# Kernel tuning notes

Hardware: AMD Instinct MI355X
Metric: run time of the kernel (lower is better)

## Reference

```python
import jax, jax.numpy as jnp
from jax import lax
import numpy as np

B, S, D, COMP = 4, 1024, 512, 4


def setup_inputs() -> dict:
    key = jax.random.key(0)
    x = jax.random.normal(key, (B * S, D), dtype=jnp.float32)
    return {"x": x, "comp_rate": COMP, "seqlen": S}


def _merge_step(x, t, seq):
    # x: [seq, D], compacted so the k = seq - t valid tokens occupy rows 0..k-1.
    xn = jnp.roll(x, -1, axis=0)  # x[i+1] (wrap value never selected among valid pairs)
    # dist only feeds argmax (non-differentiable), mirror torch exactly; stop_gradient
    # keeps the vjp from saving residuals for this dead-for-gradients path.
    xg = lax.stop_gradient(x)
    dist = jnp.sum(xg * jnp.roll(xg, -1, axis=0), axis=-1)  # scalar_product metric
    j = jnp.arange(x.shape[0])
    dist = jnp.where(j < seq - 1 - t, dist, -jnp.inf)  # k-1 valid adjacent pairs
    mid = jnp.argmax(dist)
    jm = j[:, None]
    # rows < mid keep, row mid becomes (x[mid]+x[mid+1])/2, rows > mid shift left by 1
    return jnp.where(jm < mid, x, jnp.where(jm == mid, (x + xn) * 0.5, xn))


def _merge_sample(x, steps, seq):
    def body(carry, t):
        return _merge_step(carry, t, seq), None
    x, _ = lax.scan(body, x, jnp.arange(steps))
    return x


def reference(x, comp_rate, seqlen):
    d = x.shape[-1]
    b = x.shape[0] // seqlen
    n_comp = seqlen // comp_rate
    steps = seqlen - n_comp
    xb = x.reshape(b, seqlen, d)
    merged = jax.vmap(lambda xs: _merge_sample(xs, steps, seqlen))(xb)
    # torch smart_merge concatenates per-sample results along dim 0
    return merged[:, :n_comp].reshape(b * n_comp, d)
```

## Files before the change

kernel.cpp:

```cpp
#include <hip/hip_runtime.h>
#include <math.h>

#define S 1024
#define D 512
#define NCOMP (S / 4)
#define STEPS (S - NCOMP)
#define NEG_INF (-__builtin_inff())

__device__ __forceinline__ int   f2i(float x) { return __builtin_bit_cast(int, x); }
__device__ __forceinline__ float i2f(int x)   { return __builtin_bit_cast(float, x); }
__device__ __forceinline__ int   rfl(int x)   { return __builtin_amdgcn_readfirstlane(x); }

__device__ __forceinline__ unsigned fkey(float f) {
    unsigned u = __builtin_bit_cast(unsigned, f);
    return (u & 0x80000000u) ? ~u : (u | 0x80000000u);
}

__device__ __forceinline__ float wave_sum63(float x) {
    x += i2f(__builtin_amdgcn_update_dpp(0, f2i(x), 0x111, 0xF, 0xF, true));
    x += i2f(__builtin_amdgcn_update_dpp(0, f2i(x), 0x112, 0xF, 0xF, true));
    x += i2f(__builtin_amdgcn_update_dpp(0, f2i(x), 0x114, 0xF, 0xF, true));
    x += i2f(__builtin_amdgcn_update_dpp(0, f2i(x), 0x118, 0xF, 0xF, true));
    x += i2f(__builtin_amdgcn_update_dpp(0, f2i(x), 0x142, 0xA, 0xF, true));
    x += i2f(__builtin_amdgcn_update_dpp(0, f2i(x), 0x143, 0xC, 0xF, true));
    return x;
}

__device__ __forceinline__ unsigned wave_max63(unsigned x) {
#define MAXD(c, rm) { unsigned o_ = (unsigned)__builtin_amdgcn_update_dpp(0, (int)x, (c), (rm), 0xF, true); x = (x > o_) ? x : o_; }
    MAXD(0x111, 0xF) MAXD(0x112, 0xF) MAXD(0x114, 0xF)
    MAXD(0x118, 0xF) MAXD(0x142, 0xA) MAXD(0x143, 0xC)
#undef MAXD
    return x;
}

struct Row { float4 a, b; };

__device__ __forceinline__ Row row_load(const float* vals, int slot, int lane) {
    const float4* p = (const float4*)(vals + (size_t)slot * D);
    Row r; r.a = p[lane * 2]; r.b = p[lane * 2 + 1]; return r;
}
__device__ __forceinline__ void row_store(float* vals, int slot, int lane, Row r) {
    float4* p = (float4*)(vals + (size_t)slot * D);
    p[lane * 2] = r.a; p[lane * 2 + 1] = r.b;
}
__device__ __forceinline__ Row row_avg(Row x, Row y) {
    Row r;
    r.a.x = (x.a.x + y.a.x) * 0.5f; r.a.y = (x.a.y + y.a.y) * 0.5f;
    r.a.z = (x.a.z + y.a.z) * 0.5f; r.a.w = (x.a.w + y.a.w) * 0.5f;
    r.b.x = (x.b.x + y.b.x) * 0.5f; r.b.y = (x.b.y + y.b.y) * 0.5f;
    r.b.z = (x.b.z + y.b.z) * 0.5f; r.b.w = (x.b.w + y.b.w) * 0.5f;
    return r;
}
__device__ __forceinline__ float dot8_partial(Row x, Row y) {
    float acc = x.a.x * y.a.x;
    acc += x.a.y * y.a.y; acc += x.a.z * y.a.z; acc += x.a.w * y.a.w;
    acc += x.b.x * y.b.x; acc += x.b.y * y.b.y; acc += x.b.z * y.b.z; acc += x.b.w * y.b.w;
    return acc;
}
__device__ __forceinline__ int lsr(int s) { return ((unsigned)s < (unsigned)S) ? s : 0; }
__device__ __forceinline__ int lsl(int s) { return ((unsigned)s <= (unsigned)S) ? s : 0; }

__device__ __forceinline__ void tree16k(const unsigned (&av)[16], unsigned& cm, int& ca) {
    unsigned v8[8]; int k8[8];
#pragma unroll
    for (int k = 0; k < 8; ++k) { bool tk = av[k+8] > av[k]; v8[k] = tk ? av[k+8] : av[k]; k8[k] = tk ? (k+8) : k; }
    unsigned v4[4]; int k4[4];
#pragma unroll
    for (int k = 0; k < 4; ++k) { bool tk = v8[k+4] > v8[k]; v4[k] = tk ? v8[k+4] : v8[k]; k4[k] = tk ? k8[k+4] : k8[k]; }
    unsigned v2[2]; int k2[2];
#pragma unroll
    for (int k = 0; k < 2; ++k) { bool tk = v4[k+2] > v4[k]; v2[k] = tk ? v4[k+2] : v4[k]; k2[k] = tk ? k4[k+2] : k4[k]; }
    bool tk1 = v2[1] > v2[0];
    cm = tk1 ? v2[1] : v2[0];
    ca = tk1 ? k2[1] : k2[0];
}

__device__ __forceinline__ void upd(unsigned (&av)[16], int lane, int slot, unsigned key) {
    if (lane == (slot >> 4)) {
        switch (slot & 15) {
            case 0:  av[0]  = key; break;  case 1:  av[1]  = key; break;
            case 2:  av[2]  = key; break;  case 3:  av[3]  = key; break;
            case 4:  av[4]  = key; break;  case 5:  av[5]  = key; break;
            case 6:  av[6]  = key; break;  case 7:  av[7]  = key; break;
            case 8:  av[8]  = key; break;  case 9:  av[9]  = key; break;
            case 10: av[10] = key; break;  case 11: av[11] = key; break;
            case 12: av[12] = key; break;  case 13: av[13] = key; break;
            case 14: av[14] = key; break;  case 15: av[15] = key; break;
        }
    }
}

__global__ __launch_bounds__(256) void init_kernel(const float* __restrict__ x,
                                                   float* __restrict__ vals,
                                                   float* __restrict__ out) {
    const int blk = blockIdx.x, b = blk >> 4, g = blk & 15;
    const int tid = threadIdx.x, lane = tid & 63, w = tid >> 6;
    const float* xb = x + (size_t)b * S * D;
    if (vals != x) {
        float* vb = vals + (size_t)b * S * D;
        const float4* s4 = (const float4*)xb;
        float4* d4 = (float4*)vb;
        const int base = g * (S * D / 4 / 16);
        for (int i = tid; i < S * D / 4 / 16; i += 256) d4[base + i] = s4[base + i];
    }
    float* sd = out + (size_t)b * NCOMP * D;
#pragma unroll 1
    for (int j = 0; j < 16; ++j) {
        int pr = g * 64 + w * 16 + j;
        if (pr < S - 1) {
            Row A = row_load(xb, pr, lane);
            Row B = row_load(xb, pr + 1, lane);
            float t = wave_sum63(dot8_partial(A, B));
            if (lane == 63) sd[pr] = t;
        }
    }
    if (g == 0 && tid == 0) sd[S - 1] = NEG_INF;
}

__global__ __launch_bounds__(64, 1) void merge_kernel(float* __restrict__ vals,
                                                      float* __restrict__ out) {
    const int b = blockIdx.x, lane = threadIdx.x;
    float* vb = vals + (size_t)b * S * D;
    float* aux = out + (size_t)b * NCOMP * D;
    int* outIdx = (int*)(aux + S);

    __shared__ int4 links[S + 1];
    for (int s = lane; s <= S; s += 64)
        links[s] = (s >= S) ? make_int4(S, S, S, 0)
                            : make_int4(s - 1, s + 1, (s + 2 <= S) ? (s + 2) : S, 0);

    unsigned av[16];
    {
        const float4* sd4 = (const float4*)aux;
#pragma unroll
        for (int j = 0; j < 4; ++j) {
            float4 v = sd4[lane * 4 + j];
            av[4*j+0] = fkey(v.x); av[4*j+1] = fkey(v.y);
            av[4*j+2] = fkey(v.z); av[4*j+3] = fkey(v.w);
        }
    }

    unsigned cm; int ca;
    tree16k(av, cm, ca);
    unsigned smax = (unsigned)__builtin_amdgcn_readlane((int)wave_max63(cm), 63);
    unsigned long long tied = __ballot(cm == smax);
    int wl = (int)__ffsll(tied) - 1;
    int m = rfl((wl << 4) | __builtin_amdgcn_readlane(ca, wl));
    int4 Lm = links[m];
    int p = rfl(Lm.x), r = rfl(Lm.y), q = rfl(Lm.z);
    int nq = rfl(links[lsl(q)].y);
    Row Rp = row_load(vb, lsr(p), lane);
    Row Rm = row_load(vb, m,      lane);
    Row Rr = row_load(vb, r,      lane);
    Row Rq = row_load(vb, lsr(q), lane);
    int mprev = -1;
    Row vmPrev = Rm;

#pragma unroll 1
    for (int t = 0; ; ++t) {
        const bool hasp = (p >= 0), hasq = (q < S);
        if (p == mprev) Rp = vmPrev;
        if (m == mprev) Rm = vmPrev;
        if (r == mprev) Rr = vmPrev;
        if (q == mprev) Rq = vmPrev;

        Row vm = row_avg(Rm, Rr);
        row_store(vb, m, lane, vm);

        float sp = wave_sum63(dot8_partial(Rp, vm));
        float sq = wave_sum63(dot8_partial(vm, Rq));
        unsigned ndpk = hasp ? fkey(i2f(__builtin_amdgcn_readlane(f2i(sp), 63))) : 0u;
        unsigned ndmk = hasq ? fkey(i2f(__builtin_amdgcn_readlane(f2i(sq), 63))) : 0u;

        if (lane == 0) {
            links[m].y = q; links[m].z = nq;
            if (hasp) links[p].z = q;
            if (hasq) links[q].x = m;
        }
        upd(av, lane, r, 0u);
        upd(av, lane, m, ndmk);
        if (hasp) upd(av, lane, p, ndpk);

        if (t == STEPS - 1) break;

        tree16k(av, cm, ca);
        smax = (unsigned)__builtin_amdgcn_readlane((int)wave_max63(cm), 63);
        tied = __ballot(cm == smax);
        wl = (int)__ffsll(tied) - 1;
        int m2 = rfl((wl << 4) | __builtin_amdgcn_readlane(ca, wl));

        int4 L2 = links[m2];
        int p2 = rfl(L2.x), r2 = rfl(L2.y), q2 = rfl(L2.z);
        int nq2 = rfl(links[lsl(q2)].y);
        Rp = row_load(vb, lsr(p2), lane);
        Rm = row_load(vb, m2,      lane);
        Rr = row_load(vb, r2,      lane);
        Rq = row_load(vb, lsr(q2), lane);

        mprev = m; vmPrev = vm;
        m = m2; p = p2; r = r2; q = q2; nq = nq2;
    }

    if (lane == 0) {
        int s = 0;
        for (int i = 0; i < NCOMP; i += 2) {
            int4 Ls = links[s];
            outIdx[i] = s;
            if (i + 1 < NCOMP) outIdx[i + 1] = Ls.y;
            s = Ls.z;
        }
    }
}

__global__ __launch_bounds__(256) void gather_kernel(const float* __restrict__ vals,
                                                     float* __restrict__ out) {
    const int b = blockIdx.x, part = blockIdx.y;
    const float* vb = vals + (size_t)b * S * D;
    float* ob = out + (size_t)b * NCOMP * D;
    __shared__ int oi[NCOMP / 8];
    const int row0 = part * (NCOMP / 8);
    if (threadIdx.x < NCOMP / 8)
        oi[threadIdx.x] = ((const int*)(ob + S))[row0 + threadIdx.x];
    __syncthreads();
    const float4* v4 = (const float4*)vb;
    float4* o4 = (float4*)ob;
    const int per = (NCOMP / 8) * (D / 4);
    for (int idx = threadIdx.x; idx < per; idx += 256) {
        int row = idx >> 7, c = idx & 127;
        o4[(size_t)(row0 + row) * (D / 4) + c] = v4[(size_t)oi[row] * (D / 4) + c];
    }
}

extern "C" void kernel_launch(void* const* d_in, const int* in_sizes, int n_in,
                              void* d_out, int out_size, void* d_ws, size_t ws_size,
                              hipStream_t stream) {
    const float* x = (const float*)d_in[0];
    float* out = (float*)d_out;
    const int b = in_sizes[0] / (S * D);
    const size_t need = (size_t)in_sizes[0] * sizeof(float);
    float* vals = (ws_size >= need) ? (float*)d_ws : (float*)x;
    init_kernel<<<dim3(16 * b), dim3(256), 0, stream>>>(x, vals, out);
    merge_kernel<<<dim3(b), dim3(64), 0, stream>>>(vals, out);
    gather_kernel<<<dim3(b, 8), dim3(256), 0, stream>>>(vals, out);
}
```

Baseline: 1.092 ms.

## Fuse init, merge and gather into one kernel with speculative next-merge prefetch

Merges the three launches into a single 512-thread block per sample. Adjacent-pair distances now go to shared memory instead of global memory, and the gather is done in-kernel. Inside the serial merge loop, the next argmax candidate is computed before the current update from the masked key array. The rows for that candidate and for the neighbours of the current merge are prefetched, so each step's global load latency overlaps the current step's compute. This trades more register pressure and extra speculative row loads for a shorter dependency chain per step. It also leaves only B blocks for the copy and distance phases.

```diff
diff --git a/kernel.cpp b/kernel.cpp
--- a/kernel.cpp
+++ b/kernel.cpp
@@ -91,118 +91,135 @@
     }
 }
 
-__global__ __launch_bounds__(256) void init_kernel(const float* __restrict__ x,
-                                                   float* __restrict__ vals,
-                                                   float* __restrict__ out) {
-    const int blk = blockIdx.x, b = blk >> 4, g = blk & 15;
-    const int tid = threadIdx.x, lane = tid & 63, w = tid >> 6;
+__global__ __launch_bounds__(512, 1) void pool_kernel(const float* __restrict__ x,
+                                                      float* __restrict__ out,
+                                                      float* vals_base) {
+    const int b = blockIdx.x, tid = threadIdx.x, lane = tid & 63, wave = tid >> 6;
+    float* vb = vals_base + (size_t)b * S * D;
     const float* xb = x + (size_t)b * S * D;
-    if (vals != x) {
-        float* vb = vals + (size_t)b * S * D;
+
+    __shared__ int4 links[S + 1];
+    __shared__ __align__(16) float sdist[S];
+    __shared__ int outIdx[NCOMP];
+
+    if (vals_base != x) {
         const float4* s4 = (const float4*)xb;
         float4* d4 = (float4*)vb;
-        const int base = g * (S * D / 4 / 16);
-        for (int i = tid; i < S * D / 4 / 16; i += 256) d4[base + i] = s4[base + i];
-    }
-    float* sd = out + (size_t)b * NCOMP * D;
-#pragma unroll 1
-    for (int j = 0; j < 16; ++j) {
-        int pr = g * 64 + w * 16 + j;
-        if (pr < S - 1) {
-            Row A = row_load(xb, pr, lane);
-            Row B = row_load(xb, pr + 1, lane);
-            float t = wave_sum63(dot8_partial(A, B));
-            if (lane == 63) sd[pr] = t;
-        }
-    }
-    if (g == 0 && tid == 0) sd[S - 1] = NEG_INF;
-}
-
-__global__ __launch_bounds__(64, 1) void merge_kernel(float* __restrict__ vals,
-                                                      float* __restrict__ out) {
-    const int b = blockIdx.x, lane = threadIdx.x;
-    float* vb = vals + (size_t)b * S * D;
-    float* aux = out + (size_t)b * NCOMP * D;
-    int* outIdx = (int*)(aux + S);
-
-    __shared__ int4 links[S + 1];
-    for (int s = lane; s <= S; s += 64)
+        for (int i = tid; i < S * D / 4; i += 512) d4[i] = s4[i];
+    }
+    for (int s = tid; s <= S; s += 512)
         links[s] = (s >= S) ? make_int4(S, S, S, 0)
                             : make_int4(s - 1, s + 1, (s + 2 <= S) ? (s + 2) : S, 0);
 
-    unsigned av[16];
     {
-        const float4* sd4 = (const float4*)aux;
-#pragma unroll
-        for (int j = 0; j < 4; ++j) {
-            float4 v = sd4[lane * 4 + j];
-            av[4*j+0] = fkey(v.x); av[4*j+1] = fkey(v.y);
-            av[4*j+2] = fkey(v.z); av[4*j+3] = fkey(v.w);
-        }
-    }
-
-    unsigned cm; int ca;
-    tree16k(av, cm, ca);
-    unsigned smax = (unsigned)__builtin_amdgcn_readlane((int)wave_max63(cm), 63);
-    unsigned long long tied = __ballot(cm == smax);
-    int wl = (int)__ffsll(tied) - 1;
-    int m = rfl((wl << 4) | __builtin_amdgcn_readlane(ca, wl));
-    int4 Lm = links[m];
-    int p = rfl(Lm.x), r = rfl(Lm.y), q = rfl(Lm.z);
-    int nq = rfl(links[lsl(q)].y);
-    Row Rp = row_load(vb, lsr(p), lane);
-    Row Rm = row_load(vb, m,      lane);
-    Row Rr = row_load(vb, r,      lane);
-    Row Rq = row_load(vb, lsr(q), lane);
-    int mprev = -1;
-    Row vmPrev = Rm;
-
+        const int base = wave * 128;
+        Row A = row_load(xb, base, lane);
 #pragma unroll 1
-    for (int t = 0; ; ++t) {
-        const bool hasp = (p >= 0), hasq = (q < S);
-        if (p == mprev) Rp = vmPrev;
-        if (m == mprev) Rm = vmPrev;
-        if (r == mprev) Rr = vmPrev;
-        if (q == mprev) Rq = vmPrev;
-
-        Row vm = row_avg(Rm, Rr);
-        row_store(vb, m, lane, vm);
-
-        float sp = wave_sum63(dot8_partial(Rp, vm));
-        float sq = wave_sum63(dot8_partial(vm, Rq));
-        unsigned ndpk = hasp ? fkey(i2f(__builtin_amdgcn_readlane(f2i(sp), 63))) : 0u;
-        unsigned ndmk = hasq ? fkey(i2f(__builtin_amdgcn_readlane(f2i(sq), 63))) : 0u;
-
-        if (lane == 0) {
-            links[m].y = q; links[m].z = nq;
-            if (hasp) links[p].z = q;
-            if (hasq) links[q].x = m;
-        }
-        upd(av, lane, r, 0u);
-        upd(av, lane, m, ndmk);
-        if (hasp) upd(av, lane, p, ndpk);
-
-        if (t == STEPS - 1) break;
-
+        for (int j = 0; j < 128; ++j) {
+            int idx = base + j;
+            if (idx >= S - 1) break;
+            Row B = row_load(xb, idx + 1, lane);
+            float t_ = wave_sum63(dot8_partial(A, B));
+            if (lane == 63) sdist[idx] = t_;
+            A = B;
+        }
+    }
+    __syncthreads();
+
+    if (wave == 0) {
+        unsigned av[16];
+        {
+            const float4* sd4 = (const float4*)sdist;
+#pragma unroll
+            for (int j = 0; j < 4; ++j) {
+                float4 v = sd4[lane * 4 + j];
+                av[4*j+0] = fkey(v.x); av[4*j+1] = fkey(v.y);
+                av[4*j+2] = fkey(v.z); av[4*j+3] = fkey(v.w);
+            }
+            if (lane == 63) av[15] = 0u;
+        }
+
+        unsigned cm; int ca;
         tree16k(av, cm, ca);
-        smax = (unsigned)__builtin_amdgcn_readlane((int)wave_max63(cm), 63);
-        tied = __ballot(cm == smax);
-        wl = (int)__ffsll(tied) - 1;
-        int m2 = rfl((wl << 4) | __builtin_amdgcn_readlane(ca, wl));
-
-        int4 L2 = links[m2];
-        int p2 = rfl(L2.x), r2 = rfl(L2.y), q2 = rfl(L2.z);
-        int nq2 = rfl(links[lsl(q2)].y);
-        Rp = row_load(vb, lsr(p2), lane);
-        Rm = row_load(vb, m2,      lane);
-        Rr = row_load(vb, r2,      lane);
-        Rq = row_load(vb, lsr(q2), lane);
-
-        mprev = m; vmPrev = vm;
-        m = m2; p = p2; r = r2; q = q2; nq = nq2;
-    }
-
-    if (lane == 0) {
+        unsigned smax = (unsigned)__builtin_amdgcn_readlane((int)wave_max63(cm), 63);
+        unsigned long long tied = __ballot(cm == smax);
+        int wl = (int)__ffsll(tied) - 1;
+        int m = rfl((wl << 4) | __builtin_amdgcn_readlane(ca, wl));
+        int4 Lm0 = links[m];
+        int p = rfl(Lm0.x), r = rfl(Lm0.y), q = rfl(Lm0.z);
+        int pp = (p >= 0) ? rfl(links[lsl(p)].x) : -1;
+        int nq = rfl(links[lsl(q)].y);
+        Row Rp = row_load(vb, lsr(p), lane);
+        Row Rm = row_load(vb, m,      lane);
+        Row Rr = row_load(vb, r,      lane);
+        Row Rq = row_load(vb, lsr(q), lane);
+        Row Fpp = row_load(vb, lsr(pp), lane);
+        Row Fnq = row_load(vb, lsr(nq), lane);
+
+#pragma unroll 1
+        for (int t = 0; t < STEPS; ++t) {
+            const bool hasp = (p >= 0), hasq = (q < S);
+
+            upd(av, lane, r, 0u);
+            upd(av, lane, m, 0u);
+            if (hasp) upd(av, lane, p, 0u);
+            tree16k(av, cm, ca);
+            unsigned sm1 = (unsigned)__builtin_amdgcn_readlane((int)wave_max63(cm), 63);
+            tied = __ballot(cm == sm1);
+            wl = (int)__ffsll(tied) - 1;
+            const int i1 = rfl((wl << 4) | __builtin_amdgcn_readlane(ca, wl));
+            int4 Li = links[i1];
+            int p2 = rfl(Li.x), r2 = rfl(Li.y), q2 = rfl(Li.z);
+            if (i1 == q) p2 = m;
+            Row Lp  = row_load(vb, lsr(p2), lane);
+            Row Lmr = row_load(vb, i1,      lane);
+            Row Lr  = row_load(vb, lsr(r2), lane);
+            Row Lq  = row_load(vb, lsr(q2), lane);
+
+            Row vm = row_avg(Rm, Rr);
+            row_store(vb, m, lane, vm);
+            float sp = wave_sum63(dot8_partial(Rp, vm));
+            float sq = wave_sum63(dot8_partial(vm, Rq));
+            unsigned ndpk = hasp ? fkey(i2f(__builtin_amdgcn_readlane(f2i(sp), 63))) : 0u;
+            unsigned ndmk = hasq ? fkey(i2f(__builtin_amdgcn_readlane(f2i(sq), 63))) : 0u;
+
+            if (lane == 0) {
+                links[m].y = q; links[m].z = nq;
+                if (hasp) links[p].z = q;
+                if (hasq) links[q].x = m;
+            }
+            upd(av, lane, m, ndmk);
+            if (hasp) upd(av, lane, p, ndpk);
+
+            if (t == STEPS - 1) break;
+
+            unsigned best = sm1; int bs = i1;
+            if (ndmk > best || (ndmk == best && m < bs)) { best = ndmk; bs = m; }
+            if (ndpk > best || (ndpk == best && p < bs)) { best = ndpk; bs = p; }
+            const int m2 = rfl(bs);
+
+            const int mo = m, po = p, qo = q, ppo = pp, nqo = nq;
+            if (m2 == mo) {
+                r = qo; q = nqo;
+                Rm = vm; Rr = Rq; Rq = Fnq;
+            } else if (m2 == po) {
+                m = po; p = ppo; r = mo;
+                Rm = Rp; Rr = vm; Rp = Fpp;
+            } else {
+                m = i1; p = p2; r = r2; q = q2;
+                Rm = Lmr; Rr = Lr;
+                Rp = (p2 == mo) ? vm : Lp;
+                Rq = (q2 == mo) ? vm : Lq;
+            }
+            pp = (p >= 0) ? rfl(links[lsl(p)].x) : -1;
+            nq = rfl(links[lsl(q)].y);
+            Fpp = row_load(vb, lsr(pp), lane);
+            Fnq = row_load(vb, lsr(nq), lane);
+        }
+    }
+    __syncthreads();
+
+    if (tid == 0) {
         int s = 0;
         for (int i = 0; i < NCOMP; i += 2) {
             int4 Ls = links[s];
@@ -211,24 +228,12 @@
             s = Ls.z;
         }
     }
-}
-
-__global__ __launch_bounds__(256) void gather_kernel(const float* __restrict__ vals,
-                                                     float* __restrict__ out) {
-    const int b = blockIdx.x, part = blockIdx.y;
-    const float* vb = vals + (size_t)b * S * D;
+    __syncthreads();
+
     float* ob = out + (size_t)b * NCOMP * D;
-    __shared__ int oi[NCOMP / 8];
-    const int row0 = part * (NCOMP / 8);
-    if (threadIdx.x < NCOMP / 8)
-        oi[threadIdx.x] = ((const int*)(ob + S))[row0 + threadIdx.x];
-    __syncthreads();
-    const float4* v4 = (const float4*)vb;
-    float4* o4 = (float4*)ob;
-    const int per = (NCOMP / 8) * (D / 4);
-    for (int idx = threadIdx.x; idx < per; idx += 256) {
-        int row = idx >> 7, c = idx & 127;
-        o4[(size_t)(row0 + row) * (D / 4) + c] = v4[(size_t)oi[row] * (D / 4) + c];
+    for (int i = wave; i < NCOMP; i += 8) {
+        Row rr = row_load(vb, outIdx[i], lane);
+        row_store(ob, i, lane, rr);
     }
 }
 
@@ -240,7 +245,5 @@
     const int b = in_sizes[0] / (S * D);
     const size_t need = (size_t)in_sizes[0] * sizeof(float);
     float* vals = (ws_size >= need) ? (float*)d_ws : (float*)x;
-    init_kernel<<<dim3(16 * b), dim3(256), 0, stream>>>(x, vals, out);
-    merge_kernel<<<dim3(b), dim3(64), 0, stream>>>(vals, out);
-    gather_kernel<<<dim3(b, 8), dim3(256), 0, stream>>>(vals, out);
-}
+    pool_kernel<<<dim3(b), dim3(512), 0, stream>>>(x, out, vals);
+}
```

Result: slower. 1.512 ms (+38.4%).

## Precompute distance-2 dot products so new neighbor scores come from LDS algebra

Applied to the files above, without the earlier changes.

Init now also computes dot products between rows two apart (dist2). In the merge loop, the new scores for the merged row's neighbors are taken by linearity as averages of stored dist and dist2 values, kept in LDS. This removes the two dependent wave reductions from the argmax critical path. In exchange each step does three other dot products to refresh dist2, loads six rows instead of four, and adds a two-deep forwarding cache for rows written in recent steps. Scores computed by linearity may differ slightly in rounding from direct dot products, so argmax ties could resolve differently.

```diff
diff --git a/kernel.cpp b/kernel.cpp
--- a/kernel.cpp
+++ b/kernel.cpp
@@ -10,6 +10,7 @@
 __device__ __forceinline__ int   f2i(float x) { return __builtin_bit_cast(int, x); }
 __device__ __forceinline__ float i2f(int x)   { return __builtin_bit_cast(float, x); }
 __device__ __forceinline__ int   rfl(int x)   { return __builtin_amdgcn_readfirstlane(x); }
+__device__ __forceinline__ float rl63(float x) { return i2f(__builtin_amdgcn_readlane(f2i(x), 63)); }
 
 __device__ __forceinline__ unsigned fkey(float f) {
     unsigned u = __builtin_bit_cast(unsigned, f);
@@ -59,7 +60,6 @@
     return acc;
 }
 __device__ __forceinline__ int lsr(int s) { return ((unsigned)s < (unsigned)S) ? s : 0; }
-__device__ __forceinline__ int lsl(int s) { return ((unsigned)s <= (unsigned)S) ? s : 0; }
 
 __device__ __forceinline__ void tree16k(const unsigned (&av)[16], unsigned& cm, int& ca) {
     unsigned v8[8]; int k8[8];
@@ -93,7 +93,9 @@
 
 __global__ __launch_bounds__(256) void init_kernel(const float* __restrict__ x,
                                                    float* __restrict__ vals,
-                                                   float* __restrict__ out) {
+                                                   float* __restrict__ sdB,
+                                                   float* __restrict__ sd2B,
+                                                   int stride) {
     const int blk = blockIdx.x, b = blk >> 4, g = blk & 15;
     const int tid = threadIdx.x, lane = tid & 63, w = tid >> 6;
     const float* xb = x + (size_t)b * S * D;
@@ -104,40 +106,58 @@
         const int base = g * (S * D / 4 / 16);
         for (int i = tid; i < S * D / 4 / 16; i += 256) d4[base + i] = s4[base + i];
     }
-    float* sd = out + (size_t)b * NCOMP * D;
+    float* sd  = sdB  + (size_t)b * stride;
+    float* sd2 = sd2B + (size_t)b * stride;
 #pragma unroll 1
     for (int j = 0; j < 16; ++j) {
         int pr = g * 64 + w * 16 + j;
         if (pr < S - 1) {
             Row A = row_load(xb, pr, lane);
             Row B = row_load(xb, pr + 1, lane);
-            float t = wave_sum63(dot8_partial(A, B));
-            if (lane == 63) sd[pr] = t;
-        }
-    }
-    if (g == 0 && tid == 0) sd[S - 1] = NEG_INF;
+            float t1 = wave_sum63(dot8_partial(A, B));
+            if (lane == 63) sd[pr] = t1;
+            if (pr < S - 2) {
+                Row C = row_load(xb, pr + 2, lane);
+                float t2 = wave_sum63(dot8_partial(A, C));
+                if (lane == 63) sd2[pr] = t2;
+            }
+        }
+    }
+    if (g == 0 && tid == 0) { sd[S-1] = NEG_INF; sd2[S-2] = NEG_INF; sd2[S-1] = NEG_INF; }
 }
 
 __global__ __launch_bounds__(64, 1) void merge_kernel(float* __restrict__ vals,
-                                                      float* __restrict__ out) {
+                                                      float* __restrict__ sdB,
+                                                      float* __restrict__ sd2B,
+                                                      float* __restrict__ idxB,
+                                                      int stride) {
     const int b = blockIdx.x, lane = threadIdx.x;
     float* vb = vals + (size_t)b * S * D;
-    float* aux = out + (size_t)b * NCOMP * D;
-    int* outIdx = (int*)(aux + S);
+    const float* sd  = sdB  + (size_t)b * stride;
+    const float* sd2 = sd2B + (size_t)b * stride;
+    int* outIdx = (int*)(idxB + (size_t)b * stride);
 
     __shared__ int4 links[S + 1];
+    __shared__ __align__(16) float dist[S];
+    __shared__ __align__(16) float dist2[S];
+
     for (int s = lane; s <= S; s += 64)
-        links[s] = (s >= S) ? make_int4(S, S, S, 0)
-                            : make_int4(s - 1, s + 1, (s + 2 <= S) ? (s + 2) : S, 0);
+        links[s] = (s >= S) ? make_int4(S, S, S, S)
+                            : make_int4(s - 1, s + 1, (s + 2 <= S) ? (s + 2) : S, s - 2);
 
     unsigned av[16];
     {
-        const float4* sd4 = (const float4*)aux;
+        const float4* sd4 = (const float4*)sd;
+        const float4* sq4 = (const float4*)sd2;
+        float4* dd  = (float4*)&dist[lane * 16];
+        float4* dd2 = (float4*)&dist2[lane * 16];
 #pragma unroll
         for (int j = 0; j < 4; ++j) {
             float4 v = sd4[lane * 4 + j];
             av[4*j+0] = fkey(v.x); av[4*j+1] = fkey(v.y);
             av[4*j+2] = fkey(v.z); av[4*j+3] = fkey(v.w);
+            dd[j] = v;
+            dd2[j] = sq4[lane * 4 + j];
         }
     }
 
@@ -148,39 +168,57 @@
     int wl = (int)__ffsll(tied) - 1;
     int m = rfl((wl << 4) | __builtin_amdgcn_readlane(ca, wl));
     int4 Lm = links[m];
-    int p = rfl(Lm.x), r = rfl(Lm.y), q = rfl(Lm.z);
-    int nq = rfl(links[lsl(q)].y);
-    Row Rp = row_load(vb, lsr(p), lane);
-    Row Rm = row_load(vb, m,      lane);
-    Row Rr = row_load(vb, r,      lane);
-    Row Rq = row_load(vb, lsr(q), lane);
-    int mprev = -1;
-    Row vmPrev = Rm;
+    int p = rfl(Lm.x), r = rfl(Lm.y), q = rfl(Lm.z), pp = rfl(Lm.w);
+    int nq = rfl(links[r].z);
+    Row Rm  = row_load(vb, m,       lane);
+    Row Rr  = row_load(vb, r,       lane);
+    Row Rp  = row_load(vb, lsr(p),  lane);
+    Row Rq  = row_load(vb, lsr(q),  lane);
+    Row Rpp = row_load(vb, lsr(pp), lane);
+    Row Rnq = row_load(vb, lsr(nq), lane);
+    int mp1 = -7, mp2 = -8;
+    Row vp1 = Rm, vp2 = Rm;
 
 #pragma unroll 1
-    for (int t = 0; ; ++t) {
+    for (int t = 0; t < STEPS; ++t) {
         const bool hasp = (p >= 0), hasq = (q < S);
-        if (p == mprev) Rp = vmPrev;
-        if (m == mprev) Rm = vmPrev;
-        if (r == mprev) Rr = vmPrev;
-        if (q == mprev) Rq = vmPrev;
+        const bool haspp = (pp >= 0), hasnq = (nq < S);
+
+        float d_p  = dist[lsr(p)];
+        float d2_p = dist2[lsr(p)];
+        float d2_m = dist2[m];
+        float d_r  = dist[r];
+        float ndp = hasp ? (d_p + d2_p) * 0.5f : NEG_INF;
+        float ndm = hasq ? (d2_m + d_r) * 0.5f : NEG_INF;
+        if (lane == 0) {
+            if (hasp) dist[p] = ndp;
+            dist[m] = ndm;
+        }
+        upd(av, lane, r, 0u);
+        upd(av, lane, m, hasq ? fkey(ndm) : 0u);
+        if (hasp) upd(av, lane, p, fkey(ndp));
 
         Row vm = row_avg(Rm, Rr);
         row_store(vb, m, lane, vm);
 
-        float sp = wave_sum63(dot8_partial(Rp, vm));
-        float sq = wave_sum63(dot8_partial(vm, Rq));
-        unsigned ndpk = hasp ? fkey(i2f(__builtin_amdgcn_readlane(f2i(sp), 63))) : 0u;
-        unsigned ndmk = hasq ? fkey(i2f(__builtin_amdgcn_readlane(f2i(sq), 63))) : 0u;
+        float s1 = wave_sum63(dot8_partial(Rpp, vm));
+        float s2 = wave_sum63(dot8_partial(Rp, Rq));
+        float s3 = wave_sum63(dot8_partial(vm, Rnq));
+        float d2pp = haspp ? rl63(s1) : NEG_INF;
+        float d2p  = (hasp && hasq) ? rl63(s2) : NEG_INF;
+        float d2m  = hasnq ? rl63(s3) : NEG_INF;
+        if (lane == 0) {
+            if (haspp) dist2[pp] = d2pp;
+            if (hasp)  dist2[p]  = d2p;
+            dist2[m] = d2m;
+        }
 
         if (lane == 0) {
             links[m].y = q; links[m].z = nq;
             if (hasp) links[p].z = q;
-            if (hasq) links[q].x = m;
-        }
-        upd(av, lane, r, 0u);
-        upd(av, lane, m, ndmk);
-        if (hasp) upd(av, lane, p, ndpk);
+            if (hasq) { links[q].x = m; links[q].w = p; }
+            if (hasnq) links[nq].w = m;
+        }
 
         if (t == STEPS - 1) break;
 
@@ -188,18 +226,27 @@
         smax = (unsigned)__builtin_amdgcn_readlane((int)wave_max63(cm), 63);
         tied = __ballot(cm == smax);
         wl = (int)__ffsll(tied) - 1;
-        int m2 = rfl((wl << 4) | __builtin_amdgcn_readlane(ca, wl));
+        const int m2 = rfl((wl << 4) | __builtin_amdgcn_readlane(ca, wl));
 
         int4 L2 = links[m2];
-        int p2 = rfl(L2.x), r2 = rfl(L2.y), q2 = rfl(L2.z);
-        int nq2 = rfl(links[lsl(q2)].y);
-        Rp = row_load(vb, lsr(p2), lane);
-        Rm = row_load(vb, m2,      lane);
-        Rr = row_load(vb, r2,      lane);
-        Rq = row_load(vb, lsr(q2), lane);
-
-        mprev = m; vmPrev = vm;
-        m = m2; p = p2; r = r2; q = q2; nq = nq2;
+        int p2 = rfl(L2.x), r2 = rfl(L2.y), q2 = rfl(L2.z), pp2 = rfl(L2.w);
+        int nq2 = rfl(links[r2].z);
+        Row Nm  = row_load(vb, m2,        lane);
+        Row Nr  = row_load(vb, lsr(r2),   lane);
+        Row Np  = row_load(vb, lsr(p2),   lane);
+        Row Nq  = row_load(vb, lsr(q2),   lane);
+        Row Npp = row_load(vb, lsr(pp2),  lane);
+        Row Nnq = row_load(vb, lsr(nq2),  lane);
+        if (m2 == m) Nm = vm; else if (m2 == mp1) Nm = vp1; else if (m2 == mp2) Nm = vp2;
+        if (r2 == m) Nr = vm; else if (r2 == mp1) Nr = vp1; else if (r2 == mp2) Nr = vp2;
+        if (p2 == m) Np = vm; else if (p2 == mp1) Np = vp1; else if (p2 == mp2) Np = vp2;
+        if (q2 == m) Nq = vm; else if (q2 == mp1) Nq = vp1; else if (q2 == mp2) Nq = vp2;
+        if (pp2 == m) Npp = vm; else if (pp2 == mp1) Npp = vp1; else if (pp2 == mp2) Npp = vp2;
+        if (nq2 == m) Nnq = vm; else if (nq2 == mp1) Nnq = vp1; else if (nq2 == mp2) Nnq = vp2;
+
+        mp2 = mp1; vp2 = vp1; mp1 = m; vp1 = vm;
+        m = m2; p = p2; r = r2; q = q2; pp = pp2; nq = nq2;
+        Rm = Nm; Rr = Nr; Rp = Np; Rq = Nq; Rpp = Npp; Rnq = Nnq;
     }
 
     if (lane == 0) {
@@ -214,20 +261,22 @@
 }
 
 __global__ __launch_bounds__(256) void gather_kernel(const float* __restrict__ vals,
-                                                     float* __restrict__ out) {
+                                                     float* __restrict__ out,
+                                                     const float* __restrict__ idxB,
+                                                     int stride) {
     const int b = blockIdx.x, part = blockIdx.y;
     const float* vb = vals + (size_t)b * S * D;
     float* ob = out + (size_t)b * NCOMP * D;
+    const int* idx = (const int*)(idxB + (size_t)b * stride);
     __shared__ int oi[NCOMP / 8];
     const int row0 = part * (NCOMP / 8);
-    if (threadIdx.x < NCOMP / 8)
-        oi[threadIdx.x] = ((const int*)(ob + S))[row0 + threadIdx.x];
+    if (threadIdx.x < NCOMP / 8) oi[threadIdx.x] = idx[row0 + threadIdx.x];
     __syncthreads();
     const float4* v4 = (const float4*)vb;
     float4* o4 = (float4*)ob;
     const int per = (NCOMP / 8) * (D / 4);
-    for (int idx = threadIdx.x; idx < per; idx += 256) {
-        int row = idx >> 7, c = idx & 127;
+    for (int i = threadIdx.x; i < per; i += 256) {
+        int row = i >> 7, c = i & 127;
         o4[(size_t)(row0 + row) * (D / 4) + c] = v4[(size_t)oi[row] * (D / 4) + c];
     }
 }
@@ -239,8 +288,19 @@
     float* out = (float*)d_out;
     const int b = in_sizes[0] / (S * D);
     const size_t need = (size_t)in_sizes[0] * sizeof(float);
-    float* vals = (ws_size >= need) ? (float*)d_ws : (float*)x;
-    init_kernel<<<dim3(16 * b), dim3(256), 0, stream>>>(x, vals, out);
-    merge_kernel<<<dim3(b), dim3(64), 0, stream>>>(vals, out);
-    gather_kernel<<<dim3(b, 8), dim3(256), 0, stream>>>(vals, out);
-}
+    float* vals; float *sdB, *sd2B, *idxB; int stride;
+    if (ws_size >= need + (size_t)b * 3 * S * sizeof(float)) {
+        vals = (float*)d_ws;
+        float* stage = vals + (size_t)b * S * D;
+        sdB = stage; sd2B = stage + S; idxB = stage + 2 * S; stride = 3 * S;
+    } else if (ws_size >= need) {
+        vals = (float*)d_ws;
+        sdB = out; sd2B = out + NCOMP * D - S; idxB = out + S; stride = NCOMP * D;
+    } else {
+        vals = (float*)x;
+        sdB = out; sd2B = out + NCOMP * D - S; idxB = out + S; stride = NCOMP * D;
+    }
+    init_kernel<<<dim3(16 * b), dim3(256), 0, stream>>>(x, vals, sdB, sd2B, stride);
+    merge_kernel<<<dim3(b), dim3(64), 0, stream>>>(vals, sdB, sd2B, idxB, stride);
+    gather_kernel<<<dim3(b, 8), dim3(256), 0, stream>>>(vals, out, idxB, stride);
+}
```

Result: slower. 1.460 ms (+33.6%).
